# Kernel optimization log

Hardware: AMD Instinct MI355X
Metric: run time of the kernel (lower is better)

## Reference

```python
import jax, jax.numpy as jnp
import numpy as np

B, P, S, D, DFF, VOCAB, T = 16, 16, 512, 256, 1024, 5000, 256
EPS = 1e-6

def _layernorm(x, g, b):
    mu = jnp.mean(x, axis=-1, keepdims=True)
    var = jnp.var(x, axis=-1, keepdims=True)
    return (x - mu) * jax.lax.rsqrt(var + EPS) * g + b

def setup_inputs() -> dict:
    key = jax.random.key(0)
    ks = jax.random.split(key, 16)
    nrm = lambda k, shape: (jax.random.normal(k, shape) * 0.02).astype(jnp.float32)
    return {
        'x': jax.random.normal(ks[0], (B, P, D), jnp.float32),
        'y': jax.random.randint(ks[1], (B, P, 1), 0, VOCAB),
        'K': jax.random.normal(ks[2], (B, P, S, D), jnp.float32),
        'V': jax.random.normal(ks[3], (B, P, S, D), jnp.float32),
        'R': jax.random.normal(ks[4], (B, P, S, D), jnp.float32),
        'wq': nrm(ks[5], (D, D)), 'bq': jnp.zeros((D,), jnp.float32),
        'wk': nrm(ks[6], (D, D)), 'bk': jnp.zeros((D,), jnp.float32),
        'wv': nrm(ks[7], (D, D)), 'bv': jnp.zeros((D,), jnp.float32),
        'wo': nrm(ks[8], (D, D)), 'bo': jnp.zeros((D,), jnp.float32),
        'w1': nrm(ks[9], (D, DFF)), 'b1': jnp.zeros((DFF,), jnp.float32),
        'w2': nrm(ks[10], (DFF, D)), 'b2': jnp.zeros((D,), jnp.float32),
        'ln1_g': jnp.ones((D,), jnp.float32), 'ln1_b': jnp.zeros((D,), jnp.float32),
        'ln2_g': jnp.ones((D,), jnp.float32), 'ln2_b': jnp.zeros((D,), jnp.float32),
        'w_out': nrm(ks[11], (D, VOCAB)),
        'sigmas': jnp.array([0.1, 0.1, 0.1, 0.1], jnp.float32),  # sigma_q, sigma_k, sigma_v, sigma_z
        'timestep': T,
    }

def reference(x, y, K, V, R, wq, bq, wk, bk, wv, bv, wo, bo, w1, b1, w2, b2,
              ln1_g, ln1_b, ln2_g, ln2_b, w_out, sigmas, timestep):
    t = timestep
    xq = x[:, :, None, :]                                   # (B,P,1,D)
    q_ = xq @ wq + bq
    k_ = xq @ wk + bk
    v_ = xq @ wv + bv
    nk = jax.random.split(jax.random.key(1234), 5)
    # SMC reparameterized gaussian noise on q,k,v
    q = q_ + sigmas[0] * jax.random.normal(nk[0], q_.shape, q_.dtype)
    k = k_ + sigmas[1] * jax.random.normal(nk[1], k_.shape, k_.dtype)
    v = v_ + sigmas[2] * jax.random.normal(nk[2], v_.shape, v_.dtype)
    noise_q = q - q_
    # write current k,v into timestep slot (== concat(past, k, future))
    K = K.at[:, :, t:t + 1, :].set(k)
    V = V.at[:, :, t:t + 1, :].set(v)
    Kw, Vw = K[:, :, :t + 1, :], V[:, :, :t + 1, :]         # causal window
    logits = jnp.einsum('bpqd,bpsd->bpqs', q, Kw) / jnp.sqrt(jnp.float32(D))
    attn = jax.nn.softmax(logits, axis=-1)                  # (B,P,1,t+1)
    z_ = jnp.einsum('bpqs,bpsd->bpqd', attn, Vw) @ wo + bo
    z = z_ + sigmas[3] * jax.random.normal(nk[3], z_.shape, z_.dtype)
    noise_z = z - z_
    out = _layernorm(z + xq, ln1_g, ln1_b)
    f = jax.nn.relu(out @ w1 + b1) @ w2 + b2
    r = _layernorm(f + out, ln2_g, ln2_b)                   # (B,P,1,D)
    preds = r @ w_out                                       # (B,P,1,VOCAB)
    R = R.at[:, :, t:t + 1, :].set(r)
    # particle weights (classification) + ancestor sampling
    probas = jax.nn.softmax(preds, axis=-1)[:, :, 0, :]     # (B,P,VOCAB)
    w = jnp.take_along_axis(probas, y, axis=-1)[:, :, 0]    # (B,P)
    w_norm = jax.lax.stop_gradient(jax.nn.softmax(w, axis=-1))
    i_t = jax.random.categorical(nk[4], w_norm[:, None, :], shape=(B, P))  # (B,P)
    def resample(params):
        past = jnp.take_along_axis(params[:, :, :t + 1, :], i_t[:, :, None, None], axis=1)
        return jnp.concatenate([past, params[:, :, t + 1:, :]], axis=2)
    K, V, R = resample(K), resample(V), resample(R)
    return (r, attn, noise_q, noise_z, K, V, R)
```

## Files before the change

### kernel.cpp

```cpp
#include <hip/hip_runtime.h>
#include <stdint.h>
#include <stddef.h>


#define B_    16
#define P_    16
#define S_    512
#define D_    256
#define DFF_  1024
#define VOCAB_ 5000
#define T_    256
#define ROWS_ 256
#define EPS_  1e-6f

#define PARTITIONABLE 1

__host__ __device__ __forceinline__ uint32_t rotl32_(uint32_t x, int d) {
  return (x << d) | (x >> (32 - d));
}

__host__ __device__ __forceinline__ void threefry2x32_(uint32_t k0, uint32_t k1,
                                                       uint32_t x0, uint32_t x1,
                                                       uint32_t& o0, uint32_t& o1) {
  uint32_t ks2 = k0 ^ k1 ^ 0x1BD11BDAu;
  x0 += k0; x1 += k1;
  x0 += x1; x1 = rotl32_(x1, 13); x1 ^= x0;
  x0 += x1; x1 = rotl32_(x1, 15); x1 ^= x0;
  x0 += x1; x1 = rotl32_(x1, 26); x1 ^= x0;
  x0 += x1; x1 = rotl32_(x1,  6); x1 ^= x0;
  x0 += k1; x1 += ks2 + 1u;
  x0 += x1; x1 = rotl32_(x1, 17); x1 ^= x0;
  x0 += x1; x1 = rotl32_(x1, 29); x1 ^= x0;
  x0 += x1; x1 = rotl32_(x1, 16); x1 ^= x0;
  x0 += x1; x1 = rotl32_(x1, 24); x1 ^= x0;
  x0 += ks2; x1 += k0 + 2u;
  x0 += x1; x1 = rotl32_(x1, 13); x1 ^= x0;
  x0 += x1; x1 = rotl32_(x1, 15); x1 ^= x0;
  x0 += x1; x1 = rotl32_(x1, 26); x1 ^= x0;
  x0 += x1; x1 = rotl32_(x1,  6); x1 ^= x0;
  x0 += k0; x1 += k1 + 3u;
  x0 += x1; x1 = rotl32_(x1, 17); x1 ^= x0;
  x0 += x1; x1 = rotl32_(x1, 29); x1 ^= x0;
  x0 += x1; x1 = rotl32_(x1, 16); x1 ^= x0;
  x0 += x1; x1 = rotl32_(x1, 24); x1 ^= x0;
  x0 += k1; x1 += ks2 + 4u;
  x0 += x1; x1 = rotl32_(x1, 13); x1 ^= x0;
  x0 += x1; x1 = rotl32_(x1, 15); x1 ^= x0;
  x0 += x1; x1 = rotl32_(x1, 26); x1 ^= x0;
  x0 += x1; x1 = rotl32_(x1,  6); x1 ^= x0;
  x0 += ks2; x1 += k0 + 5u;
  o0 = x0; o1 = x1;
}

__device__ __forceinline__ uint32_t jax_bits(uint32_t k0, uint32_t k1,
                                             uint32_t i) {
#if PARTITIONABLE
  uint32_t o0, o1;
  threefry2x32_(k0, k1, 0u, i, o0, o1);
  return o0 ^ o1;
#else
  return 0u;
#endif
}

__device__ __forceinline__ float bits_to_u01(uint32_t b) {
  return __uint_as_float((b >> 9) | 0x3F800000u) - 1.0f;
}

__device__ __forceinline__ float erfinv32(float x) {
  float w = -log1pf(-x * x);
  float p;
  if (w < 5.0f) {
    w -= 2.5f;
    p = 2.81022636e-08f;
    p = fmaf(p, w, 3.43273939e-07f);
    p = fmaf(p, w, -3.5233877e-06f);
    p = fmaf(p, w, -4.39150654e-06f);
    p = fmaf(p, w, 0.00021858087f);
    p = fmaf(p, w, -0.00125372503f);
    p = fmaf(p, w, -0.00417768164f);
    p = fmaf(p, w, 0.246640727f);
    p = fmaf(p, w, 1.50140941f);
  } else {
    w = sqrtf(w) - 3.0f;
    p = -0.000200214257f;
    p = fmaf(p, w, 0.000100950558f);
    p = fmaf(p, w, 0.00134934322f);
    p = fmaf(p, w, -0.00367342844f);
    p = fmaf(p, w, 0.00573950773f);
    p = fmaf(p, w, -0.0076224613f);
    p = fmaf(p, w, 0.00943887047f);
    p = fmaf(p, w, 1.00167406f);
    p = fmaf(p, w, 2.83297682f);
  }
  return p * x;
}

__device__ __forceinline__ float jax_normal(uint32_t k0, uint32_t k1,
                                            uint32_t i) {
  float u01 = bits_to_u01(jax_bits(k0, k1, i));
  const float lo = -0.99999994f;
  float u = __fadd_rn(__fmul_rn(u01, 2.0f), lo);
  u = fmaxf(lo, u);
  return 1.41421356f * erfinv32(u);
}

__device__ __forceinline__ float jax_gumbel(uint32_t k0, uint32_t k1,
                                            uint32_t i) {
  float u01 = bits_to_u01(jax_bits(k0, k1, i));
  const float tiny = 1.17549435e-38f;
  float u = __fadd_rn(__fmul_rn(u01, 1.0f), tiny);
  u = fmaxf(tiny, u);
  return -logf(-logf(u));
}

__device__ __forceinline__ float blk_sum(float v, float* red, int tid) {
  #pragma unroll
  for (int off = 32; off > 0; off >>= 1) v += __shfl_xor(v, off, 64);
  if ((tid & 63) == 0) red[tid >> 6] = v;
  __syncthreads();
  if (tid == 0) {
    float s = 0.f;
    #pragma unroll
    for (int i = 0; i < 16; i++) s += red[i];
    red[16] = s;
  }
  __syncthreads();
  float r = red[16];
  __syncthreads();
  return r;
}
__device__ __forceinline__ float blk_max(float v, float* red, int tid) {
  #pragma unroll
  for (int off = 32; off > 0; off >>= 1) v = fmaxf(v, __shfl_xor(v, off, 64));
  if ((tid & 63) == 0) red[tid >> 6] = v;
  __syncthreads();
  if (tid == 0) {
    float s = -INFINITY;
    #pragma unroll
    for (int i = 0; i < 16; i++) s = fmaxf(s, red[i]);
    red[16] = s;
  }
  __syncthreads();
  float r = red[16];
  __syncthreads();
  return r;
}

__global__ __launch_bounds__(1024) void fused_row_kernel(
    const float* __restrict__ x,
    const float* __restrict__ Kin, const float* __restrict__ Vin,
    const float* __restrict__ wq, const float* __restrict__ bq,
    const float* __restrict__ wk, const float* __restrict__ bk,
    const float* __restrict__ wv, const float* __restrict__ bv,
    const float* __restrict__ wo, const float* __restrict__ bo,
    const float* __restrict__ w1, const float* __restrict__ b1,
    const float* __restrict__ w2, const float* __restrict__ b2,
    const float* __restrict__ ln1g, const float* __restrict__ ln1b,
    const float* __restrict__ ln2g, const float* __restrict__ ln2b,
    const float* __restrict__ sigmas,
    float* __restrict__ kws, float* __restrict__ vws,
    float* __restrict__ attn_out, float* __restrict__ noiseq_out,
    float* __restrict__ noisez_out, float* __restrict__ r_out,
    uint32_t kq0, uint32_t kq1, uint32_t kk0, uint32_t kk1,
    uint32_t kv0, uint32_t kv1, uint32_t kz0, uint32_t kz1) {
  __shared__ __align__(16) float xs[D_], qs[D_], ksh[D_], vsh[D_], z0s[D_], os[D_];
  __shared__ float att[T_ + 4];
  __shared__ __align__(16) float hs[DFF_];
  __shared__ float4 scq[16][64];
  __shared__ float4 sck[16][64];
  __shared__ float4 scv[16][64];
  __shared__ float red[32];
  const int row = blockIdx.x, t = threadIdx.x;
  const int cg = t & 63;
  const int sl = t >> 6;

  if (t < D_) xs[t] = x[row * D_ + t];
  __syncthreads();

  {
    const float4* wqf = (const float4*)wq;
    const float4* wkf = (const float4*)wk;
    const float4* wvf = (const float4*)wv;
    float4 aq = {0,0,0,0}, ak = {0,0,0,0}, av = {0,0,0,0};
    const int e0 = sl * 16;
    #pragma unroll
    for (int e = e0; e < e0 + 16; e++) {
      float xe = xs[e];
      float4 a = wqf[e * 64 + cg];
      float4 b = wkf[e * 64 + cg];
      float4 c = wvf[e * 64 + cg];
      aq.x = fmaf(xe, a.x, aq.x); aq.y = fmaf(xe, a.y, aq.y);
      aq.z = fmaf(xe, a.z, aq.z); aq.w = fmaf(xe, a.w, aq.w);
      ak.x = fmaf(xe, b.x, ak.x); ak.y = fmaf(xe, b.y, ak.y);
      ak.z = fmaf(xe, b.z, ak.z); ak.w = fmaf(xe, b.w, ak.w);
      av.x = fmaf(xe, c.x, av.x); av.y = fmaf(xe, c.y, av.y);
      av.z = fmaf(xe, c.z, av.z); av.w = fmaf(xe, c.w, av.w);
    }
    scq[sl][cg] = aq; sck[sl][cg] = ak; scv[sl][cg] = av;
  }
  __syncthreads();
  if (t < 768) {
    const int m = t >> 8, c = t & 255;
    const float* sc = (m == 0) ? (const float*)scq
                    : (m == 1) ? (const float*)sck : (const float*)scv;
    float s = 0.f;
    #pragma unroll
    for (int j = 0; j < 16; j++) s += sc[j * 256 + c];
    float bias = ((m == 0) ? bq : (m == 1) ? bk : bv)[c];
    float base = bias + s;
    uint32_t i = (uint32_t)row * D_ + c;
    uint32_t a0 = (m == 0) ? kq0 : (m == 1) ? kk0 : kv0;
    uint32_t a1 = (m == 0) ? kq1 : (m == 1) ? kk1 : kv1;
    float val = base + sigmas[m] * jax_normal(a0, a1, i);
    if (m == 0)      { qs[c] = val; noiseq_out[i] = val - base; }
    else if (m == 1) { ksh[c] = val; kws[i] = val; }
    else             { vsh[c] = val; vws[i] = val; }
  }
  __syncthreads();

  {
    const int sq = t >> 2;
    const int qp = t & 3;
    const float4* qf4 = (const float4*)qs;
    const float4* Krow = (const float4*)(Kin + ((size_t)row * S_ + sq) * D_);
    float rr = 0.f;
    #pragma unroll
    for (int j = 0; j < 16; j++) {
      float4 k4 = Krow[j * 4 + qp];
      float4 q4 = qf4[j * 4 + qp];
      rr += q4.x * k4.x + q4.y * k4.y + q4.z * k4.z + q4.w * k4.w;
    }
    rr += __shfl_xor(rr, 1, 64);
    rr += __shfl_xor(rr, 2, 64);
    if (qp == 0) att[sq] = rr * 0.0625f;
    if (t < 64) {
      float4 k4 = ((const float4*)ksh)[t];
      float4 q4 = qf4[t];
      float r2 = q4.x * k4.x + q4.y * k4.y + q4.z * k4.z + q4.w * k4.w;
      #pragma unroll
      for (int off = 32; off > 0; off >>= 1) r2 += __shfl_xor(r2, off, 64);
      if (t == 0) att[T_] = r2 * 0.0625f;
    }
  }
  __syncthreads();

  {
    float v = (t <= T_) ? att[t] : -INFINITY;
    float mx = blk_max(v, red, t);
    float e = (t <= T_) ? expf(att[t] - mx) : 0.f;
    float sum = blk_sum(e, red, t);
    if (t <= T_) {
      float a = e / sum;
      att[t] = a;
      attn_out[(size_t)row * (T_ + 1) + t] = a;
    }
  }
  __syncthreads();

  {
    const float4* Vf = (const float4*)(Vin + (size_t)row * S_ * D_);
    float4 acc = {0,0,0,0};
    const int s0 = sl * 16;
    #pragma unroll
    for (int s = s0; s < s0 + 16; s++) {
      float a = att[s];
      float4 v4 = Vf[s * 64 + cg];
      acc.x = fmaf(a, v4.x, acc.x); acc.y = fmaf(a, v4.y, acc.y);
      acc.z = fmaf(a, v4.z, acc.z); acc.w = fmaf(a, v4.w, acc.w);
    }
    scq[sl][cg] = acc;
  }
  __syncthreads();
  if (t < D_) {
    float s = 0.f;
    #pragma unroll
    for (int j = 0; j < 16; j++) s += ((const float*)scq)[j * 256 + t];
    z0s[t] = s + att[T_] * vsh[t];
  }
  __syncthreads();

  {
    const float4* wof = (const float4*)wo;
    float4 acc = {0,0,0,0};
    const int e0 = sl * 16;
    #pragma unroll
    for (int e = e0; e < e0 + 16; e++) {
      float ze = z0s[e];
      float4 w4 = wof[e * 64 + cg];
      acc.x = fmaf(ze, w4.x, acc.x); acc.y = fmaf(ze, w4.y, acc.y);
      acc.z = fmaf(ze, w4.z, acc.z); acc.w = fmaf(ze, w4.w, acc.w);
    }
    sck[sl][cg] = acc;
  }
  __syncthreads();
  if (t < D_) {
    float s = 0.f;
    #pragma unroll
    for (int j = 0; j < 16; j++) s += ((const float*)sck)[j * 256 + t];
    float zp = bo[t] + s;
    uint32_t i = (uint32_t)row * D_ + t;
    float zn = zp + sigmas[3] * jax_normal(kz0, kz1, i);
    noisez_out[i] = zn - zp;
    z0s[t] = zn + xs[t];
  }
  __syncthreads();
  {
    float y = (t < D_) ? z0s[t] : 0.f;
    float mu = blk_sum(y, red, t) * (1.0f / 256.0f);
    float dv = (t < D_) ? (z0s[t] - mu) : 0.f;
    float var = blk_sum(dv * dv, red, t) * (1.0f / 256.0f);
    if (t < D_) os[t] = dv * rsqrtf(var + EPS_) * ln1g[t] + ln1b[t];
  }
  __syncthreads();

  {
    const int cg8 = t & 255, es = t >> 8;
    const float4* w1f = (const float4*)w1;
    float4 acc = {0,0,0,0};
    const int e0 = es * 64;
    #pragma unroll 8
    for (int e = e0; e < e0 + 64; e++) {
      float oe = os[e];
      float4 w4 = w1f[e * 256 + cg8];
      acc.x = fmaf(oe, w4.x, acc.x); acc.y = fmaf(oe, w4.y, acc.y);
      acc.z = fmaf(oe, w4.z, acc.z); acc.w = fmaf(oe, w4.w, acc.w);
    }
    ((float4*)scq)[es * 256 + cg8] = acc;
  }
  __syncthreads();
  {
    float s = 0.f;
    #pragma unroll
    for (int j = 0; j < 4; j++) s += ((const float*)scq)[j * 1024 + t];
    hs[t] = fmaxf(b1[t] + s, 0.f);
  }
  __syncthreads();

  {
    const float4* w2f = (const float4*)w2;
    float4 acc = {0,0,0,0};
    const int e0 = sl * 64;
    #pragma unroll 8
    for (int e = e0; e < e0 + 64; e++) {
      float he = hs[e];
      float4 w4 = w2f[e * 64 + cg];
      acc.x = fmaf(he, w4.x, acc.x); acc.y = fmaf(he, w4.y, acc.y);
      acc.z = fmaf(he, w4.z, acc.z); acc.w = fmaf(he, w4.w, acc.w);
    }
    scv[sl][cg] = acc;
  }
  __syncthreads();
  if (t < D_) {
    float s = 0.f;
    #pragma unroll
    for (int j = 0; j < 16; j++) s += ((const float*)scv)[j * 256 + t];
    z0s[t] = b2[t] + s + os[t];
  }
  __syncthreads();
  {
    float y = (t < D_) ? z0s[t] : 0.f;
    float mu = blk_sum(y, red, t) * (1.0f / 256.0f);
    float dv = (t < D_) ? (z0s[t] - mu) : 0.f;
    float var = blk_sum(dv * dv, red, t) * (1.0f / 256.0f);
    if (t < D_)
      r_out[(size_t)row * D_ + t] = dv * rsqrtf(var + EPS_) * ln2g[t] + ln2b[t];
  }
}

#define PREDS_BLOCKS 320
#define TAIL_BLOCKS_PER_TENSOR 1020
__global__ __launch_bounds__(256) void preds_tail_kernel(
    const float* __restrict__ r, const float* __restrict__ w_out,
    const int* __restrict__ y,
    const float4* __restrict__ Kin, const float4* __restrict__ Vin,
    const float4* __restrict__ Rin,
    float4* __restrict__ Kout, float4* __restrict__ Vout,
    float4* __restrict__ Rout,
    float* __restrict__ pm, float* __restrict__ ps, float* __restrict__ pe) {
  const int bx = blockIdx.x, tid = threadIdx.x;
  if (bx >= PREDS_BLOCKS) {
    const int c = bx - PREDS_BLOCKS;
    const int tau = c / TAIL_BLOCKS_PER_TENSOR;
    const int c2 = c - tau * TAIL_BLOCKS_PER_TENSOR;
    const uint32_t s = 257u + (uint32_t)(c2 >> 2);
    const uint32_t q = (uint32_t)(c2 & 3);
    const float4* in = (tau == 0) ? Kin : (tau == 1) ? Vin : Rin;
    float4* out      = (tau == 0) ? Kout : (tau == 1) ? Vout : Rout;
    #pragma unroll
    for (int k = 0; k < 16; k++) {
      uint32_t local = (uint32_t)k * 256u + (uint32_t)tid;
      uint32_t bp = (q << 6) | (local >> 6);
      uint32_t d4 = local & 63u;
      uint32_t f4i = (bp << 15) | (s << 6) | d4;
      out[f4i] = in[f4i];
    }
    return;
  }
  __shared__ float sm[16][264];
  __shared__ float pr16[16][17];
  __shared__ float pms[16], pss[16], eys[16];
  __shared__ int yvs[16];
  const int rc = bx / 20, cc = bx - rc * 20;
  const int rb = rc * 16;
  const int col = cc * 250 + tid;
  const int colc = (col < VOCAB_) ? col : (VOCAB_ - 1);
  if (tid < 16) { yvs[tid] = y[rb + tid]; eys[tid] = 0.f; }
  float acc[16];
  #pragma unroll
  for (int m = 0; m < 16; m++) acc[m] = 0.f;
  #pragma unroll 4
  for (int e = 0; e < D_; e++) {
    float wv = w_out[(size_t)e * VOCAB_ + colc];
    #pragma unroll
    for (int m = 0; m < 16; m++)
      acc[m] = fmaf(r[(size_t)(rb + m) * D_ + e], wv, acc[m]);
  }
  const bool act = (tid < 250);
  #pragma unroll
  for (int m = 0; m < 16; m++) sm[m][tid] = act ? acc[m] : -INFINITY;
  __syncthreads();
  {
    const int rr = tid >> 4, j = tid & 15;
    float mx = -INFINITY;
    for (int c = j; c < 256; c += 16) mx = fmaxf(mx, sm[rr][c]);
    pr16[rr][j] = mx;
  }
  __syncthreads();
  if (tid < 16) {
    float mx = -INFINITY;
    #pragma unroll
    for (int j = 0; j < 16; j++) mx = fmaxf(mx, pr16[tid][j]);
    pms[tid] = mx;
  }
  __syncthreads();
  {
    const int rr = tid >> 4, j = tid & 15;
    float mb = pms[rr];
    float sum = 0.f;
    for (int c = j; c < 256; c += 16) sum += expf(sm[rr][c] - mb);
    pr16[rr][j] = sum;
  }
  __syncthreads();
  if (tid < 16) {
    float s = 0.f;
    #pragma unroll
    for (int j = 0; j < 16; j++) s += pr16[tid][j];
    pss[tid] = s;
  }
  __syncthreads();
  if (act) {
    #pragma unroll
    for (int m = 0; m < 16; m++)
      if (col == yvs[m]) eys[m] = expf(acc[m] - pms[m]);
  }
  __syncthreads();
  if (tid < 16) {
    pm[(rb + tid) * 20 + cc] = pms[tid];
    ps[(rb + tid) * 20 + cc] = pss[tid];
    pe[(rb + tid) * 20 + cc] = eys[tid];
  }
}

__global__ __launch_bounds__(256) void combine_cat_kernel(
    const float* __restrict__ pm, const float* __restrict__ ps,
    const float* __restrict__ pe, int* __restrict__ i_t,
    uint32_t kc0, uint32_t kc1) {
  __shared__ float wv[256];
  __shared__ float wn[256];
  const int tid = threadIdx.x;
  {
    float M = -INFINITY;
    #pragma unroll 4
    for (int c = 0; c < 20; c++) M = fmaxf(M, pm[tid * 20 + c]);
    float S = 0.f, E = 0.f;
    #pragma unroll 4
    for (int c = 0; c < 20; c++) {
      float sc = expf(pm[tid * 20 + c] - M);
      S += ps[tid * 20 + c] * sc;
      E += pe[tid * 20 + c] * sc;
    }
    wv[tid] = E / S;
  }
  __syncthreads();
  const int b = tid >> 4;
  float mx = -INFINITY;
  for (int j = 0; j < 16; j++) mx = fmaxf(mx, wv[b * 16 + j]);
  float ev = expf(wv[tid] - mx);
  wn[tid] = ev;
  __syncthreads();
  float sum = 0.f;
  for (int j = 0; j < 16; j++) sum += wn[b * 16 + j];
  __syncthreads();
  wn[tid] = ev / sum;
  __syncthreads();
  float best = -INFINITY;
  int bi = 0;
  for (int j = 0; j < 16; j++) {
    uint32_t idx = (uint32_t)tid * 16u + (uint32_t)j;
    float g = jax_gumbel(kc0, kc1, idx);
    float sc = g + wn[b * 16 + j];
    if (sc > best) { best = sc; bi = j; }
  }
  i_t[tid] = bi;
}

#define HEAD_F4_PER_BP 16448u
__global__ __launch_bounds__(256) void head_resample_kernel(
    const float4* __restrict__ Kin, const float4* __restrict__ Vin,
    const float4* __restrict__ Rin,
    const float4* __restrict__ knew, const float4* __restrict__ vnew,
    const float4* __restrict__ rnew,
    const int* __restrict__ i_t,
    float4* __restrict__ Kout, float4* __restrict__ Vout,
    float4* __restrict__ Rout) {
  uint32_t idx = blockIdx.x * 256u + threadIdx.x;
  uint32_t bp = idx / HEAD_F4_PER_BP;
  uint32_t rrem = idx - bp * HEAD_F4_PER_BP;
  uint32_t s = rrem >> 6, d4 = rrem & 63u;
  const float4* in; const float4* nw; float4* out;
  if (blockIdx.y == 0)      { in = Kin; nw = knew; out = Kout; }
  else if (blockIdx.y == 1) { in = Vin; nw = vnew; out = Vout; }
  else                      { in = Rin; nw = rnew; out = Rout; }
  uint32_t ip = (uint32_t)i_t[bp];
  uint32_t srcbp = (bp & ~15u) | ip;
  float4 val;
  if (s == T_) val = nw[(srcbp << 6) | d4];
  else         val = in[(srcbp << 15) | (s << 6) | d4];
  out[(bp << 15) | (s << 6) | d4] = val;
}

static void compute_subkeys(uint32_t nk[5][2]) {
  const uint32_t k0 = 0u, k1 = 1234u;
  for (uint32_t j = 0; j < 5; j++)
    threefry2x32_(k0, k1, 0u, j, nk[j][0], nk[j][1]);
}

extern "C" void kernel_launch(void* const* d_in, const int* in_sizes, int n_in,
                              void* d_out, int out_size, void* d_ws, size_t ws_size,
                              hipStream_t stream) {
  const float* x    = (const float*)d_in[0];
  const int*   y    = (const int*)d_in[1];
  const float* Kin  = (const float*)d_in[2];
  const float* Vin  = (const float*)d_in[3];
  const float* Rin  = (const float*)d_in[4];
  const float* wq   = (const float*)d_in[5];  const float* bq = (const float*)d_in[6];
  const float* wk   = (const float*)d_in[7];  const float* bk = (const float*)d_in[8];
  const float* wv   = (const float*)d_in[9];  const float* bv = (const float*)d_in[10];
  const float* wo   = (const float*)d_in[11]; const float* bo = (const float*)d_in[12];
  const float* w1   = (const float*)d_in[13]; const float* b1 = (const float*)d_in[14];
  const float* w2   = (const float*)d_in[15]; const float* b2 = (const float*)d_in[16];
  const float* ln1g = (const float*)d_in[17]; const float* ln1b = (const float*)d_in[18];
  const float* ln2g = (const float*)d_in[19]; const float* ln2b = (const float*)d_in[20];
  const float* w_out = (const float*)d_in[21];
  const float* sigmas = (const float*)d_in[22];
  (void)in_sizes; (void)n_in; (void)out_size; (void)ws_size;

  float* out        = (float*)d_out;
  float* r_out      = out;
  float* attn_out   = out + 65536;
  float* noiseq_out = out + 131328;
  float* noisez_out = out + 196864;
  float* K_out      = out + 262400;
  float* V_out      = out + 33816832;
  float* R_out      = out + 67371264;

  float* wsf  = (float*)d_ws;
  float* kws  = wsf;
  float* vws  = wsf + 65536;
  float* pm   = wsf + 131072;
  float* ps   = wsf + 136192;
  float* pe   = wsf + 141312;
  int*   i_t  = (int*)(wsf + 146432);

  uint32_t nk[5][2];
  compute_subkeys(nk);

  fused_row_kernel<<<ROWS_, 1024, 0, stream>>>(
      x, Kin, Vin, wq, bq, wk, bk, wv, bv, wo, bo, w1, b1, w2, b2,
      ln1g, ln1b, ln2g, ln2b, sigmas,
      kws, vws, attn_out, noiseq_out, noisez_out, r_out,
      nk[0][0], nk[0][1], nk[1][0], nk[1][1], nk[2][0], nk[2][1],
      nk[3][0], nk[3][1]);
  preds_tail_kernel<<<PREDS_BLOCKS + 3 * TAIL_BLOCKS_PER_TENSOR, 256, 0, stream>>>(
      r_out, w_out, y,
      (const float4*)Kin, (const float4*)Vin, (const float4*)Rin,
      (float4*)K_out, (float4*)V_out, (float4*)R_out,
      pm, ps, pe);
  combine_cat_kernel<<<1, 256, 0, stream>>>(pm, ps, pe, i_t,
                                            nk[4][0], nk[4][1]);
  head_resample_kernel<<<dim3(16448, 3), 256, 0, stream>>>(
      (const float4*)Kin, (const float4*)Vin, (const float4*)Rin,
      (const float4*)kws, (const float4*)vws, (const float4*)r_out,
      i_t, (float4*)K_out, (float4*)V_out, (float4*)R_out);
}
```

Baseline: 256.7 us.

## Move K/V/R future-slot copy into the row kernel to overlap with compute

```diff
diff --git a/kernel.cpp b/kernel.cpp
--- a/kernel.cpp
+++ b/kernel.cpp
@@ -147,7 +147,7 @@
   return r;
 }
 
-__global__ __launch_bounds__(1024) void fused_row_kernel(
+__global__ __launch_bounds__(1024) void fused_tail_kernel(
     const float* __restrict__ x,
     const float* __restrict__ Kin, const float* __restrict__ Vin,
     const float* __restrict__ wq, const float* __restrict__ bq,
@@ -162,6 +162,9 @@
     float* __restrict__ kws, float* __restrict__ vws,
     float* __restrict__ attn_out, float* __restrict__ noiseq_out,
     float* __restrict__ noisez_out, float* __restrict__ r_out,
+    const float4* __restrict__ Rin4,
+    float4* __restrict__ Kout, float4* __restrict__ Vout,
+    float4* __restrict__ Rout,
     uint32_t kq0, uint32_t kq1, uint32_t kk0, uint32_t kk1,
     uint32_t kv0, uint32_t kv1, uint32_t kz0, uint32_t kz1) {
   __shared__ __align__(16) float xs[D_], qs[D_], ksh[D_], vsh[D_], z0s[D_], os[D_];
@@ -171,7 +174,33 @@
   __shared__ float4 sck[16][64];
   __shared__ float4 scv[16][64];
   __shared__ float red[32];
-  const int row = blockIdx.x, t = threadIdx.x;
+  const int bid = blockIdx.x, t = threadIdx.x;
+
+  if ((bid & 3) != 0) {
+    const int c = bid - (bid >> 2) - 1;
+    if (c >= 765) return;
+    const int tau = c / 255;
+    const uint32_t s = 257u + (uint32_t)(c - tau * 255);
+    const float4* in = (tau == 0) ? (const float4*)Kin
+                     : (tau == 1) ? (const float4*)Vin : Rin4;
+    float4* outp     = (tau == 0) ? Kout : (tau == 1) ? Vout : Rout;
+    #pragma unroll
+    for (int h = 0; h < 2; h++) {
+      float4 v[8]; uint32_t dst[8];
+      #pragma unroll
+      for (int k = 0; k < 8; k++) {
+        uint32_t local = (uint32_t)(h * 8 + k) * 1024u + (uint32_t)t;
+        uint32_t bp = local >> 6, d4 = local & 63u;
+        uint32_t f4i = (bp << 15) | (s << 6) | d4;
+        v[k] = in[f4i]; dst[k] = f4i;
+      }
+      #pragma unroll
+      for (int k = 0; k < 8; k++) outp[dst[k]] = v[k];
+    }
+    return;
+  }
+
+  const int row = bid >> 2;
   const int cg = t & 63;
   const int sl = t >> 6;
 
@@ -189,13 +218,13 @@
       float xe = xs[e];
       float4 a = wqf[e * 64 + cg];
       float4 b = wkf[e * 64 + cg];
-      float4 c = wvf[e * 64 + cg];
+      float4 c4 = wvf[e * 64 + cg];
       aq.x = fmaf(xe, a.x, aq.x); aq.y = fmaf(xe, a.y, aq.y);
       aq.z = fmaf(xe, a.z, aq.z); aq.w = fmaf(xe, a.w, aq.w);
       ak.x = fmaf(xe, b.x, ak.x); ak.y = fmaf(xe, b.y, ak.y);
       ak.z = fmaf(xe, b.z, ak.z); ak.w = fmaf(xe, b.w, ak.w);
-      av.x = fmaf(xe, c.x, av.x); av.y = fmaf(xe, c.y, av.y);
-      av.z = fmaf(xe, c.z, av.z); av.w = fmaf(xe, c.w, av.w);
+      av.x = fmaf(xe, c4.x, av.x); av.y = fmaf(xe, c4.y, av.y);
+      av.z = fmaf(xe, c4.z, av.z); av.w = fmaf(xe, c4.w, av.w);
     }
     scq[sl][cg] = aq; sck[sl][cg] = ak; scv[sl][cg] = av;
   }
@@ -368,39 +397,15 @@
   }
 }
 
-#define PREDS_BLOCKS 320
-#define TAIL_BLOCKS_PER_TENSOR 1020
-__global__ __launch_bounds__(256) void preds_tail_kernel(
+__global__ __launch_bounds__(256) void preds_kernel(
     const float* __restrict__ r, const float* __restrict__ w_out,
     const int* __restrict__ y,
-    const float4* __restrict__ Kin, const float4* __restrict__ Vin,
-    const float4* __restrict__ Rin,
-    float4* __restrict__ Kout, float4* __restrict__ Vout,
-    float4* __restrict__ Rout,
     float* __restrict__ pm, float* __restrict__ ps, float* __restrict__ pe) {
-  const int bx = blockIdx.x, tid = threadIdx.x;
-  if (bx >= PREDS_BLOCKS) {
-    const int c = bx - PREDS_BLOCKS;
-    const int tau = c / TAIL_BLOCKS_PER_TENSOR;
-    const int c2 = c - tau * TAIL_BLOCKS_PER_TENSOR;
-    const uint32_t s = 257u + (uint32_t)(c2 >> 2);
-    const uint32_t q = (uint32_t)(c2 & 3);
-    const float4* in = (tau == 0) ? Kin : (tau == 1) ? Vin : Rin;
-    float4* out      = (tau == 0) ? Kout : (tau == 1) ? Vout : Rout;
-    #pragma unroll
-    for (int k = 0; k < 16; k++) {
-      uint32_t local = (uint32_t)k * 256u + (uint32_t)tid;
-      uint32_t bp = (q << 6) | (local >> 6);
-      uint32_t d4 = local & 63u;
-      uint32_t f4i = (bp << 15) | (s << 6) | d4;
-      out[f4i] = in[f4i];
-    }
-    return;
-  }
   __shared__ float sm[16][264];
   __shared__ float pr16[16][17];
   __shared__ float pms[16], pss[16], eys[16];
   __shared__ int yvs[16];
+  const int bx = blockIdx.x, tid = threadIdx.x;
   const int rc = bx / 20, cc = bx - rc * 20;
   const int rb = rc * 16;
   const int col = cc * 250 + tid;
@@ -576,17 +581,15 @@
   uint32_t nk[5][2];
   compute_subkeys(nk);
 
-  fused_row_kernel<<<ROWS_, 1024, 0, stream>>>(
+  fused_tail_kernel<<<1024, 1024, 0, stream>>>(
       x, Kin, Vin, wq, bq, wk, bk, wv, bv, wo, bo, w1, b1, w2, b2,
       ln1g, ln1b, ln2g, ln2b, sigmas,
       kws, vws, attn_out, noiseq_out, noisez_out, r_out,
+      (const float4*)Rin,
+      (float4*)K_out, (float4*)V_out, (float4*)R_out,
       nk[0][0], nk[0][1], nk[1][0], nk[1][1], nk[2][0], nk[2][1],
       nk[3][0], nk[3][1]);
-  preds_tail_kernel<<<PREDS_BLOCKS + 3 * TAIL_BLOCKS_PER_TENSOR, 256, 0, stream>>>(
-      r_out, w_out, y,
-      (const float4*)Kin, (const float4*)Vin, (const float4*)Rin,
-      (float4*)K_out, (float4*)V_out, (float4*)R_out,
-      pm, ps, pe);
+  preds_kernel<<<320, 256, 0, stream>>>(r_out, w_out, y, pm, ps, pe);
   combine_cat_kernel<<<1, 256, 0, stream>>>(pm, ps, pe, i_t,
                                             nk[4][0], nk[4][1]);
   head_resample_kernel<<<dim3(16448, 3), 256, 0, stream>>>(
```

Result: slower. 383.9 us (+49.6%).

## Split fused row kernel into QKV, attention and batched MLP kernels

Applied to the files above, without the earlier changes.

```diff
diff --git a/kernel.cpp b/kernel.cpp
--- a/kernel.cpp
+++ b/kernel.cpp
@@ -12,8 +12,6 @@
 #define T_    256
 #define ROWS_ 256
 #define EPS_  1e-6f
-
-#define PARTITIONABLE 1
 
 __host__ __device__ __forceinline__ uint32_t rotl32_(uint32_t x, int d) {
   return (x << d) | (x >> (32 - d));
@@ -54,13 +52,9 @@
 
 __device__ __forceinline__ uint32_t jax_bits(uint32_t k0, uint32_t k1,
                                              uint32_t i) {
-#if PARTITIONABLE
   uint32_t o0, o1;
   threefry2x32_(k0, k1, 0u, i, o0, o1);
   return o0 ^ o1;
-#else
-  return 0u;
-#endif
 }
 
 __device__ __forceinline__ float bits_to_u01(uint32_t b) {
@@ -146,82 +140,95 @@
   __syncthreads();
   return r;
 }
-
-__global__ __launch_bounds__(1024) void fused_row_kernel(
+__device__ __forceinline__ float grp_sum256(float v, float* red16, int t) {
+  #pragma unroll
+  for (int off = 32; off > 0; off >>= 1) v += __shfl_xor(v, off, 64);
+  const int w = t >> 6;
+  if ((t & 63) == 0) red16[w] = v;
+  __syncthreads();
+  const int g = t >> 8;
+  float s = red16[g * 4] + red16[g * 4 + 1] + red16[g * 4 + 2] + red16[g * 4 + 3];
+  __syncthreads();
+  return s;
+}
+
+#define TAIL_BLOCKS_PER_TENSOR 1020
+__global__ __launch_bounds__(256) void tail_copy_kernel(
+    const float4* __restrict__ Kin, const float4* __restrict__ Vin,
+    const float4* __restrict__ Rin,
+    float4* __restrict__ Kout, float4* __restrict__ Vout,
+    float4* __restrict__ Rout) {
+  const int c = blockIdx.x, tid = threadIdx.x;
+  const int tau = c / TAIL_BLOCKS_PER_TENSOR;
+  const int c2 = c - tau * TAIL_BLOCKS_PER_TENSOR;
+  const uint32_t s = 257u + (uint32_t)(c2 >> 2);
+  const uint32_t q = (uint32_t)(c2 & 3);
+  const float4* in = (tau == 0) ? Kin : (tau == 1) ? Vin : Rin;
+  float4* out      = (tau == 0) ? Kout : (tau == 1) ? Vout : Rout;
+  #pragma unroll
+  for (int k = 0; k < 16; k++) {
+    uint32_t local = (uint32_t)k * 256u + (uint32_t)tid;
+    uint32_t bp = (q << 6) | (local >> 6);
+    uint32_t d4 = local & 63u;
+    uint32_t f4i = (bp << 15) | (s << 6) | d4;
+    out[f4i] = in[f4i];
+  }
+}
+
+__global__ __launch_bounds__(1024) void qkv_kernel(
     const float* __restrict__ x,
-    const float* __restrict__ Kin, const float* __restrict__ Vin,
     const float* __restrict__ wq, const float* __restrict__ bq,
     const float* __restrict__ wk, const float* __restrict__ bk,
     const float* __restrict__ wv, const float* __restrict__ bv,
-    const float* __restrict__ wo, const float* __restrict__ bo,
-    const float* __restrict__ w1, const float* __restrict__ b1,
-    const float* __restrict__ w2, const float* __restrict__ b2,
-    const float* __restrict__ ln1g, const float* __restrict__ ln1b,
-    const float* __restrict__ ln2g, const float* __restrict__ ln2b,
     const float* __restrict__ sigmas,
-    float* __restrict__ kws, float* __restrict__ vws,
-    float* __restrict__ attn_out, float* __restrict__ noiseq_out,
-    float* __restrict__ noisez_out, float* __restrict__ r_out,
+    float* __restrict__ qws, float* __restrict__ kws, float* __restrict__ vws,
+    float* __restrict__ noiseq_out,
     uint32_t kq0, uint32_t kq1, uint32_t kk0, uint32_t kk1,
-    uint32_t kv0, uint32_t kv1, uint32_t kz0, uint32_t kz1) {
-  __shared__ __align__(16) float xs[D_], qs[D_], ksh[D_], vsh[D_], z0s[D_], os[D_];
+    uint32_t kv0, uint32_t kv1) {
+  __shared__ float xs[4][D_];
+  const int t = threadIdx.x;
+  const int rr = t >> 8, c = t & 255;
+  const int row = blockIdx.x * 4 + rr;
+  xs[rr][c] = x[row * D_ + c];
+  __syncthreads();
+  float aq = 0.f, ak = 0.f, av = 0.f;
+  #pragma unroll 8
+  for (int e = 0; e < D_; e++) {
+    float xe = xs[rr][e];
+    aq = fmaf(xe, wq[e * D_ + c], aq);
+    ak = fmaf(xe, wk[e * D_ + c], ak);
+    av = fmaf(xe, wv[e * D_ + c], av);
+  }
+  const uint32_t i = (uint32_t)row * D_ + c;
+  const float bq_ = bq[c] + aq, bk_ = bk[c] + ak, bv_ = bv[c] + av;
+  const float qn = bq_ + sigmas[0] * jax_normal(kq0, kq1, i);
+  const float kn = bk_ + sigmas[1] * jax_normal(kk0, kk1, i);
+  const float vn = bv_ + sigmas[2] * jax_normal(kv0, kv1, i);
+  qws[i] = qn; kws[i] = kn; vws[i] = vn;
+  noiseq_out[i] = qn - bq_;
+}
+
+__global__ __launch_bounds__(1024) void attn_kernel(
+    const float* __restrict__ Kin, const float* __restrict__ Vin,
+    const float* __restrict__ qws, const float* __restrict__ kws,
+    const float* __restrict__ vws,
+    float* __restrict__ attn_out, float* __restrict__ z0ws) {
+  __shared__ __align__(16) float qs[D_], ksh[D_], vsh[D_];
   __shared__ float att[T_ + 4];
-  __shared__ __align__(16) float hs[DFF_];
   __shared__ float4 scq[16][64];
-  __shared__ float4 sck[16][64];
-  __shared__ float4 scv[16][64];
   __shared__ float red[32];
   const int row = blockIdx.x, t = threadIdx.x;
-  const int cg = t & 63;
-  const int sl = t >> 6;
-
-  if (t < D_) xs[t] = x[row * D_ + t];
-  __syncthreads();
-
-  {
-    const float4* wqf = (const float4*)wq;
-    const float4* wkf = (const float4*)wk;
-    const float4* wvf = (const float4*)wv;
-    float4 aq = {0,0,0,0}, ak = {0,0,0,0}, av = {0,0,0,0};
-    const int e0 = sl * 16;
-    #pragma unroll
-    for (int e = e0; e < e0 + 16; e++) {
-      float xe = xs[e];
-      float4 a = wqf[e * 64 + cg];
-      float4 b = wkf[e * 64 + cg];
-      float4 c = wvf[e * 64 + cg];
-      aq.x = fmaf(xe, a.x, aq.x); aq.y = fmaf(xe, a.y, aq.y);
-      aq.z = fmaf(xe, a.z, aq.z); aq.w = fmaf(xe, a.w, aq.w);
-      ak.x = fmaf(xe, b.x, ak.x); ak.y = fmaf(xe, b.y, ak.y);
-      ak.z = fmaf(xe, b.z, ak.z); ak.w = fmaf(xe, b.w, ak.w);
-      av.x = fmaf(xe, c.x, av.x); av.y = fmaf(xe, c.y, av.y);
-      av.z = fmaf(xe, c.z, av.z); av.w = fmaf(xe, c.w, av.w);
-    }
-    scq[sl][cg] = aq; sck[sl][cg] = ak; scv[sl][cg] = av;
-  }
-  __syncthreads();
-  if (t < 768) {
-    const int m = t >> 8, c = t & 255;
-    const float* sc = (m == 0) ? (const float*)scq
-                    : (m == 1) ? (const float*)sck : (const float*)scv;
-    float s = 0.f;
-    #pragma unroll
-    for (int j = 0; j < 16; j++) s += sc[j * 256 + c];
-    float bias = ((m == 0) ? bq : (m == 1) ? bk : bv)[c];
-    float base = bias + s;
-    uint32_t i = (uint32_t)row * D_ + c;
-    uint32_t a0 = (m == 0) ? kq0 : (m == 1) ? kk0 : kv0;
-    uint32_t a1 = (m == 0) ? kq1 : (m == 1) ? kk1 : kv1;
-    float val = base + sigmas[m] * jax_normal(a0, a1, i);
-    if (m == 0)      { qs[c] = val; noiseq_out[i] = val - base; }
-    else if (m == 1) { ksh[c] = val; kws[i] = val; }
-    else             { vsh[c] = val; vws[i] = val; }
-  }
-  __syncthreads();
-
-  {
-    const int sq = t >> 2;
-    const int qp = t & 3;
+  const int cg = t & 63, sl = t >> 6;
+
+  if (t < D_) {
+    qs[t] = qws[row * D_ + t];
+    ksh[t] = kws[row * D_ + t];
+    vsh[t] = vws[row * D_ + t];
+  }
+  __syncthreads();
+
+  {
+    const int sq = t >> 2, qp = t & 3;
     const float4* qf4 = (const float4*)qs;
     const float4* Krow = (const float4*)(Kin + ((size_t)row * S_ + sq) * D_);
     float rr = 0.f;
@@ -236,7 +243,7 @@
     if (qp == 0) att[sq] = rr * 0.0625f;
     if (t < 64) {
       float4 k4 = ((const float4*)ksh)[t];
-      float4 q4 = qf4[t];
+      float4 q4 = ((const float4*)qs)[t];
       float r2 = q4.x * k4.x + q4.y * k4.y + q4.z * k4.z + q4.w * k4.w;
       #pragma unroll
       for (int off = 32; off > 0; off >>= 1) r2 += __shfl_xor(r2, off, 64);
@@ -260,7 +267,7 @@
 
   {
     const float4* Vf = (const float4*)(Vin + (size_t)row * S_ * D_);
-    float4 acc = {0,0,0,0};
+    float4 acc = {0, 0, 0, 0};
     const int s0 = sl * 16;
     #pragma unroll
     for (int s = s0; s < s0 + 16; s++) {
@@ -276,131 +283,86 @@
     float s = 0.f;
     #pragma unroll
     for (int j = 0; j < 16; j++) s += ((const float*)scq)[j * 256 + t];
-    z0s[t] = s + att[T_] * vsh[t];
-  }
-  __syncthreads();
-
-  {
-    const float4* wof = (const float4*)wo;
-    float4 acc = {0,0,0,0};
-    const int e0 = sl * 16;
-    #pragma unroll
-    for (int e = e0; e < e0 + 16; e++) {
-      float ze = z0s[e];
-      float4 w4 = wof[e * 64 + cg];
-      acc.x = fmaf(ze, w4.x, acc.x); acc.y = fmaf(ze, w4.y, acc.y);
-      acc.z = fmaf(ze, w4.z, acc.z); acc.w = fmaf(ze, w4.w, acc.w);
-    }
-    sck[sl][cg] = acc;
-  }
-  __syncthreads();
-  if (t < D_) {
-    float s = 0.f;
-    #pragma unroll
-    for (int j = 0; j < 16; j++) s += ((const float*)sck)[j * 256 + t];
-    float zp = bo[t] + s;
-    uint32_t i = (uint32_t)row * D_ + t;
+    z0ws[(size_t)row * D_ + t] = s + att[T_] * vsh[t];
+  }
+}
+
+__global__ __launch_bounds__(1024) void post_kernel(
+    const float* __restrict__ x, const float* __restrict__ z0ws,
+    const float* __restrict__ wo, const float* __restrict__ bo,
+    const float* __restrict__ w1, const float* __restrict__ b1,
+    const float* __restrict__ w2, const float* __restrict__ b2,
+    const float* __restrict__ ln1g, const float* __restrict__ ln1b,
+    const float* __restrict__ ln2g, const float* __restrict__ ln2b,
+    const float* __restrict__ sigmas,
+    float* __restrict__ noisez_out, float* __restrict__ r_out,
+    uint32_t kz0, uint32_t kz1) {
+  __shared__ float z0s[4][D_];
+  __shared__ float os[4][D_];
+  __shared__ float hs[4][DFF_];
+  __shared__ float red16[16];
+  const int t = threadIdx.x;
+  const int rr = t >> 8, c = t & 255;
+  const int row = blockIdx.x * 4 + rr;
+  z0s[rr][c] = z0ws[row * D_ + c];
+  __syncthreads();
+
+  {
+    float zp = 0.f;
+    #pragma unroll 8
+    for (int e = 0; e < D_; e++) zp = fmaf(z0s[rr][e], wo[e * D_ + c], zp);
+    zp += bo[c];
+    const uint32_t i = (uint32_t)row * D_ + c;
     float zn = zp + sigmas[3] * jax_normal(kz0, kz1, i);
     noisez_out[i] = zn - zp;
-    z0s[t] = zn + xs[t];
-  }
-  __syncthreads();
-  {
-    float y = (t < D_) ? z0s[t] : 0.f;
-    float mu = blk_sum(y, red, t) * (1.0f / 256.0f);
-    float dv = (t < D_) ? (z0s[t] - mu) : 0.f;
-    float var = blk_sum(dv * dv, red, t) * (1.0f / 256.0f);
-    if (t < D_) os[t] = dv * rsqrtf(var + EPS_) * ln1g[t] + ln1b[t];
-  }
-  __syncthreads();
-
-  {
-    const int cg8 = t & 255, es = t >> 8;
-    const float4* w1f = (const float4*)w1;
-    float4 acc = {0,0,0,0};
-    const int e0 = es * 64;
+    float y = zn + x[i];
+    float mu = grp_sum256(y, red16, t) * (1.0f / 256.0f);
+    float dv = y - mu;
+    float var = grp_sum256(dv * dv, red16, t) * (1.0f / 256.0f);
+    os[rr][c] = dv * rsqrtf(var + EPS_) * ln1g[c] + ln1b[c];
+  }
+  __syncthreads();
+
+  {
+    float a0 = 0.f, a1 = 0.f, a2 = 0.f, a3 = 0.f;
     #pragma unroll 8
-    for (int e = e0; e < e0 + 64; e++) {
-      float oe = os[e];
-      float4 w4 = w1f[e * 256 + cg8];
-      acc.x = fmaf(oe, w4.x, acc.x); acc.y = fmaf(oe, w4.y, acc.y);
-      acc.z = fmaf(oe, w4.z, acc.z); acc.w = fmaf(oe, w4.w, acc.w);
+    for (int e = 0; e < D_; e++) {
+      float w = w1[(size_t)e * DFF_ + t];
+      a0 = fmaf(os[0][e], w, a0);
+      a1 = fmaf(os[1][e], w, a1);
+      a2 = fmaf(os[2][e], w, a2);
+      a3 = fmaf(os[3][e], w, a3);
     }
-    ((float4*)scq)[es * 256 + cg8] = acc;
-  }
-  __syncthreads();
-  {
-    float s = 0.f;
-    #pragma unroll
-    for (int j = 0; j < 4; j++) s += ((const float*)scq)[j * 1024 + t];
-    hs[t] = fmaxf(b1[t] + s, 0.f);
-  }
-  __syncthreads();
-
-  {
-    const float4* w2f = (const float4*)w2;
-    float4 acc = {0,0,0,0};
-    const int e0 = sl * 64;
+    float b = b1[t];
+    hs[0][t] = fmaxf(b + a0, 0.f);
+    hs[1][t] = fmaxf(b + a1, 0.f);
+    hs[2][t] = fmaxf(b + a2, 0.f);
+    hs[3][t] = fmaxf(b + a3, 0.f);
+  }
+  __syncthreads();
+
+  {
+    float acc = 0.f;
     #pragma unroll 8
-    for (int e = e0; e < e0 + 64; e++) {
-      float he = hs[e];
-      float4 w4 = w2f[e * 64 + cg];
-      acc.x = fmaf(he, w4.x, acc.x); acc.y = fmaf(he, w4.y, acc.y);
-      acc.z = fmaf(he, w4.z, acc.z); acc.w = fmaf(he, w4.w, acc.w);
-    }
-    scv[sl][cg] = acc;
-  }
-  __syncthreads();
-  if (t < D_) {
-    float s = 0.f;
-    #pragma unroll
-    for (int j = 0; j < 16; j++) s += ((const float*)scv)[j * 256 + t];
-    z0s[t] = b2[t] + s + os[t];
-  }
-  __syncthreads();
-  {
-    float y = (t < D_) ? z0s[t] : 0.f;
-    float mu = blk_sum(y, red, t) * (1.0f / 256.0f);
-    float dv = (t < D_) ? (z0s[t] - mu) : 0.f;
-    float var = blk_sum(dv * dv, red, t) * (1.0f / 256.0f);
-    if (t < D_)
-      r_out[(size_t)row * D_ + t] = dv * rsqrtf(var + EPS_) * ln2g[t] + ln2b[t];
-  }
-}
-
-#define PREDS_BLOCKS 320
-#define TAIL_BLOCKS_PER_TENSOR 1020
-__global__ __launch_bounds__(256) void preds_tail_kernel(
+    for (int e = 0; e < DFF_; e++)
+      acc = fmaf(hs[rr][e], w2[(size_t)e * D_ + c], acc);
+    float yv = b2[c] + acc + os[rr][c];
+    float mu = grp_sum256(yv, red16, t) * (1.0f / 256.0f);
+    float dv = yv - mu;
+    float var = grp_sum256(dv * dv, red16, t) * (1.0f / 256.0f);
+    r_out[(size_t)row * D_ + c] = dv * rsqrtf(var + EPS_) * ln2g[c] + ln2b[c];
+  }
+}
+
+__global__ __launch_bounds__(256) void preds_kernel(
     const float* __restrict__ r, const float* __restrict__ w_out,
     const int* __restrict__ y,
-    const float4* __restrict__ Kin, const float4* __restrict__ Vin,
-    const float4* __restrict__ Rin,
-    float4* __restrict__ Kout, float4* __restrict__ Vout,
-    float4* __restrict__ Rout,
     float* __restrict__ pm, float* __restrict__ ps, float* __restrict__ pe) {
-  const int bx = blockIdx.x, tid = threadIdx.x;
-  if (bx >= PREDS_BLOCKS) {
-    const int c = bx - PREDS_BLOCKS;
-    const int tau = c / TAIL_BLOCKS_PER_TENSOR;
-    const int c2 = c - tau * TAIL_BLOCKS_PER_TENSOR;
-    const uint32_t s = 257u + (uint32_t)(c2 >> 2);
-    const uint32_t q = (uint32_t)(c2 & 3);
-    const float4* in = (tau == 0) ? Kin : (tau == 1) ? Vin : Rin;
-    float4* out      = (tau == 0) ? Kout : (tau == 1) ? Vout : Rout;
-    #pragma unroll
-    for (int k = 0; k < 16; k++) {
-      uint32_t local = (uint32_t)k * 256u + (uint32_t)tid;
-      uint32_t bp = (q << 6) | (local >> 6);
-      uint32_t d4 = local & 63u;
-      uint32_t f4i = (bp << 15) | (s << 6) | d4;
-      out[f4i] = in[f4i];
-    }
-    return;
-  }
   __shared__ float sm[16][264];
   __shared__ float pr16[16][17];
   __shared__ float pms[16], pss[16], eys[16];
   __shared__ int yvs[16];
+  const int bx = blockIdx.x, tid = threadIdx.x;
   const int rc = bx / 20, cc = bx - rc * 20;
   const int rb = rc * 16;
   const int col = cc * 250 + tid;
@@ -566,27 +528,30 @@
   float* R_out      = out + 67371264;
 
   float* wsf  = (float*)d_ws;
-  float* kws  = wsf;
-  float* vws  = wsf + 65536;
-  float* pm   = wsf + 131072;
-  float* ps   = wsf + 136192;
-  float* pe   = wsf + 141312;
-  int*   i_t  = (int*)(wsf + 146432);
+  float* qws  = wsf;
+  float* kws  = wsf + 65536;
+  float* vws  = wsf + 131072;
+  float* z0ws = wsf + 196608;
+  float* pm   = wsf + 262144;
+  float* ps   = wsf + 267264;
+  float* pe   = wsf + 272384;
+  int*   i_t  = (int*)(wsf + 277504);
 
   uint32_t nk[5][2];
   compute_subkeys(nk);
 
-  fused_row_kernel<<<ROWS_, 1024, 0, stream>>>(
-      x, Kin, Vin, wq, bq, wk, bk, wv, bv, wo, bo, w1, b1, w2, b2,
-      ln1g, ln1b, ln2g, ln2b, sigmas,
-      kws, vws, attn_out, noiseq_out, noisez_out, r_out,
-      nk[0][0], nk[0][1], nk[1][0], nk[1][1], nk[2][0], nk[2][1],
-      nk[3][0], nk[3][1]);
-  preds_tail_kernel<<<PREDS_BLOCKS + 3 * TAIL_BLOCKS_PER_TENSOR, 256, 0, stream>>>(
-      r_out, w_out, y,
+  tail_copy_kernel<<<3 * TAIL_BLOCKS_PER_TENSOR, 256, 0, stream>>>(
       (const float4*)Kin, (const float4*)Vin, (const float4*)Rin,
-      (float4*)K_out, (float4*)V_out, (float4*)R_out,
-      pm, ps, pe);
+      (float4*)K_out, (float4*)V_out, (float4*)R_out);
+  qkv_kernel<<<64, 1024, 0, stream>>>(
+      x, wq, bq, wk, bk, wv, bv, sigmas, qws, kws, vws, noiseq_out,
+      nk[0][0], nk[0][1], nk[1][0], nk[1][1], nk[2][0], nk[2][1]);
+  attn_kernel<<<ROWS_, 1024, 0, stream>>>(
+      Kin, Vin, qws, kws, vws, attn_out, z0ws);
+  post_kernel<<<64, 1024, 0, stream>>>(
+      x, z0ws, wo, bo, w1, b1, w2, b2, ln1g, ln1b, ln2g, ln2b, sigmas,
+      noisez_out, r_out, nk[3][0], nk[3][1]);
+  preds_kernel<<<320, 256, 0, stream>>>(r_out, w_out, y, pm, ps, pe);
   combine_cat_kernel<<<1, 256, 0, stream>>>(pm, ps, pe, i_t,
                                             nk[4][0], nk[4][1]);
   head_resample_kernel<<<dim3(16448, 3), 256, 0, stream>>>(
```

Result: slower. 376.0 us (+46.5%).
